# Performance work log

Measured on AMD Instinct MI355X. Metric: run time of the kernel, lower is better.

## Reference

```python
import jax, jax.numpy as jnp
import numpy as np

N_HEADS = 16
BLOCK_SIZE = 256


def _rope(x):
    # x: [B, H, L, d] ; matches torch RotaryPositionalEmbedding (interleave-split then concat)
    B, H, L, d = x.shape
    inv_freq = 1.0 / (10000.0 ** (jnp.arange(0, d, 2, dtype=jnp.float32) / d))
    t = jnp.arange(L, dtype=jnp.float32)[:, None] * inv_freq[None, :]  # [L, d/2]
    cos, sin = jnp.cos(t), jnp.sin(t)
    x1, x2 = x[..., 0::2], x[..., 1::2]
    return jnp.concatenate([x1 * cos - x2 * sin, x2 * cos + x1 * sin], axis=-1)


def setup_inputs() -> dict:
    key = jax.random.key(0)
    k1, k2, k3 = jax.random.split(key, 3)
    B, L, D = 2, 4096, 1024
    x = jax.random.normal(k1, (B, L, D), dtype=jnp.float32)
    Wqkv = jax.random.normal(k2, (3 * D, D), dtype=jnp.float32) * 0.02
    Wout = jax.random.normal(k3, (D, D), dtype=jnp.float32) * 0.02
    return {"x": x, "Wqkv": Wqkv, "Wout": Wout}


def reference(x, Wqkv, Wout):
    H, BS = N_HEADS, BLOCK_SIZE
    B, L, D = x.shape
    HD = D // H
    scale = HD ** (-0.5)
    nb = L // BS

    qkv = (x @ Wqkv.T).reshape(B, L, 3, H, HD).transpose(2, 0, 3, 1, 4)  # [3,B,H,L,HD]
    q, k, v = qkv[0], qkv[1], qkv[2]
    q, k = _rope(q), _rope(k)

    # block-diagonal causal attention: only within-block scores are ever unmasked,
    # and fp32 exp(finfo.min - max) == 0, so blockwise softmax == masked full softmax
    qb = q.reshape(B, H, nb, BS, HD)
    kb = k.reshape(B, H, nb, BS, HD)
    vb = v.reshape(B, H, nb, BS, HD)

    att = jnp.einsum('bhnqd,bhnkd->bhnqk', qb, kb) * scale
    causal = jnp.tril(jnp.ones((BS, BS), dtype=bool))
    att = jnp.where(causal, att, jnp.finfo(att.dtype).min)
    att = jax.nn.softmax(att, axis=-1)  # dropout p=0.0 -> identity

    out = jnp.einsum('bhnqk,bhnkd->bhnqd', att, vb)
    out = out.reshape(B, H, L, HD).transpose(0, 2, 1, 3).reshape(B, L, D)
    return out @ Wout.T
```

## Files before the change

### kernel.cpp

```cpp
#include <hip/hip_runtime.h>
#include <hip/hip_bf16.h>
#include <cstdint>
#include <cstddef>

typedef __hip_bfloat16 bf16;
typedef __attribute__((ext_vector_type(8))) short bf16x8;
typedef __attribute__((ext_vector_type(4))) float floatx4;

static constexpr int Bb = 2;
static constexpr int Ls = 4096;
static constexpr int Dm = 1024;
static constexpr int Hn = 16;
static constexpr int HD = 64;
static constexpr int BS = 256;
static constexpr int QKVROW = 3 * Dm;
static constexpr int KRP = 72;

static constexpr size_t NX  = (size_t)8192 * 1024;
static constexpr size_t NQ  = (size_t)8192 * 3072;
static constexpr size_t NW1 = (size_t)3072 * 1024;
static constexpr size_t NW2 = (size_t)1024 * 1024;

__device__ __forceinline__ void async_load16(const void* g, void* l) {
  __builtin_amdgcn_global_load_lds(
      (__attribute__((address_space(1))) void*)(void*)(g),
      (__attribute__((address_space(3))) void*)(l), 16, 0, 0);
}

__device__ __forceinline__ short f2bf(float f) {
  union { __hip_bfloat16 b; short s; } u;
  u.b = __float2bfloat16(f);
  return u.s;
}

__device__ __forceinline__ float bf2f(short s) {
  union { unsigned u; float f; } v;
  v.u = ((unsigned)(unsigned short)s) << 16;
  return v.f;
}

__device__ __forceinline__ bf16x8 load8(const float* p) {
  const float4 f0 = *(const float4*)(const void*)p;
  const float4 f1 = *(const float4*)(const void*)(p + 4);
  bf16x8 r;
  r[0] = f2bf(f0.x); r[1] = f2bf(f0.y); r[2] = f2bf(f0.z); r[3] = f2bf(f0.w);
  r[4] = f2bf(f1.x); r[5] = f2bf(f1.y); r[6] = f2bf(f1.z); r[7] = f2bf(f1.w);
  return r;
}

__device__ __forceinline__ void storeC(bf16* C, size_t idx, float v) {
  C[idx] = __float2bfloat16(v);
}
__device__ __forceinline__ void storeC(float* C, size_t idx, float v) {
  C[idx] = v;
}

__global__ void cvt3_kernel(const float* __restrict__ x, const float* __restrict__ w1,
                            const float* __restrict__ w2, bf16* __restrict__ xb,
                            bf16* __restrict__ w1b, bf16* __restrict__ w2b) {
  const size_t i = ((size_t)blockIdx.x * 256 + threadIdx.x) * 8;
  if (i < NX) {
    *(bf16x8*)(void*)((short*)(void*)xb + i) = load8(x + i);
  } else if (i < NX + NW1) {
    const size_t k = i - NX;
    *(bf16x8*)(void*)((short*)(void*)w1b + k) = load8(w1 + k);
  } else {
    const size_t k = i - NX - NW1;
    *(bf16x8*)(void*)((short*)(void*)w2b + k) = load8(w2 + k);
  }
}

template <typename TC>
__global__ __launch_bounds__(512, 2) void gemm_8p(
    const bf16* __restrict__ A, const bf16* __restrict__ Bm, TC* __restrict__ C,
    int M, int N, int K) {
  constexpr int BK = 64;
  __shared__ __align__(16) short sA[3][256 * 64];
  __shared__ __align__(16) short sB[3][128 * 64];
  const int tid = threadIdx.x;
  const int wave = tid >> 6, lane = tid & 63;
  const int quad = lane >> 4, l15 = lane & 15;
  const int wr = wave >> 1, wc = wave & 1;
  const int tm = blockIdx.y * 256, tn = blockIdx.x * 128;

  const int iLo = tid >> 3;
  const int csP = tid & 7;
  const int csL = csP ^ (iLo & 7);
  const bf16* gA[4];
  const bf16* gB[2];
#pragma unroll
  for (int j = 0; j < 4; j++) gA[j] = A + (size_t)(tm + iLo + 64 * j) * K + csL * 8;
#pragma unroll
  for (int j = 0; j < 2; j++) gB[j] = Bm + (size_t)(tn + iLo + 64 * j) * K + csL * 8;

  short* aC  = &sA[0][0];
  short* aN1 = &sA[1][0];
  short* aN2 = &sA[2][0];
  short* bC  = &sB[0][0];
  short* bN1 = &sB[1][0];
  short* bN2 = &sB[2][0];

#define STH1(aD, bD, kb)                                   \
  do {                                                     \
    async_load16(gA[0] + (kb), (aD) + tid * 8);            \
    async_load16(gA[1] + (kb), (aD) + 4096 + tid * 8);     \
    async_load16(gB[0] + (kb), (bD) + tid * 8);            \
  } while (0)
#define STH2(aD, bD, kb)                                   \
  do {                                                     \
    async_load16(gA[2] + (kb), (aD) + 8192 + tid * 8);     \
    async_load16(gA[3] + (kb), (aD) + 12288 + tid * 8);    \
    async_load16(gB[1] + (kb), (bD) + 4096 + tid * 8);     \
  } while (0)
#define BARR()                                             \
  do {                                                     \
    asm volatile("" ::: "memory");                         \
    __builtin_amdgcn_s_barrier();                          \
    asm volatile("" ::: "memory");                         \
  } while (0)
#define LGKM0() asm volatile("s_waitcnt lgkmcnt(0)" ::: "memory")
#define RDB4(bP)                                                               \
  do {                                                                         \
    _Pragma("unroll") for (int n = 0; n < 4; n++)                              \
        _Pragma("unroll") for (int ks = 0; ks < 2; ks++)                       \
            bfr[n][ks] = *(const bf16x8*)((bP) + (wc * 64 + n * 16 + l15) * 64 \
                              + ((ks * 4 + quad) ^ (l15 & 7)) * 8);            \
  } while (0)
#define RDA2(aP, mh)                                                           \
  do {                                                                         \
    _Pragma("unroll") for (int mm = 0; mm < 2; mm++)                           \
        _Pragma("unroll") for (int ks = 0; ks < 2; ks++)                       \
            af[mm][ks] = *(const bf16x8*)(                                     \
                (aP) + (wr * 64 + ((mh)*2 + mm) * 16 + l15) * 64               \
                + ((ks * 4 + quad) ^ (l15 & 7)) * 8);                          \
  } while (0)
#define MM16(mh)                                                               \
  do {                                                                         \
    __builtin_amdgcn_s_setprio(1);                                             \
    _Pragma("unroll") for (int mm = 0; mm < 2; mm++)                           \
        _Pragma("unroll") for (int n = 0; n < 4; n++) {                        \
      acc[(mh)*2 + mm][n] = __builtin_amdgcn_mfma_f32_16x16x32_bf16(           \
          af[mm][0], bfr[n][0], acc[(mh)*2 + mm][n], 0, 0, 0);                 \
      acc[(mh)*2 + mm][n] = __builtin_amdgcn_mfma_f32_16x16x32_bf16(           \
          af[mm][1], bfr[n][1], acc[(mh)*2 + mm][n], 0, 0, 0);                 \
    }                                                                          \
    __builtin_amdgcn_s_setprio(0);                                             \
  } while (0)

  floatx4 acc[4][4];
#pragma unroll
  for (int i = 0; i < 4; i++)
#pragma unroll
    for (int j = 0; j < 4; j++) acc[i][j] = {0.f, 0.f, 0.f, 0.f};
  bf16x8 af[2][2], bfr[4][2];

  const int nk = K / BK;

  STH1(aC, bC, 0);
  STH2(aC, bC, 0);
  STH1(aN1, bN1, BK);
  STH2(aN1, bN1, BK);
  asm volatile("s_waitcnt vmcnt(6)" ::: "memory");
  BARR();

  for (int t = 0; t < nk - 2; ++t) {
    const int kb2 = (t + 2) * BK;
    RDB4(bC);
    RDA2(aC, 0);
    STH1(aN2, bN2, kb2);
    BARR();
    LGKM0();
    MM16(0);
    BARR();
    RDA2(aC, 1);
    STH2(aN2, bN2, kb2);
    asm volatile("s_waitcnt vmcnt(6)" ::: "memory");
    BARR();
    LGKM0();
    MM16(1);
    BARR();
    short* ta = aC; aC = aN1; aN1 = aN2; aN2 = ta;
    short* tb = bC; bC = bN1; bN1 = bN2; bN2 = tb;
  }
  RDB4(bC);
  RDA2(aC, 0);
  BARR();
  LGKM0();
  MM16(0);
  BARR();
  RDA2(aC, 1);
  asm volatile("s_waitcnt vmcnt(0)" ::: "memory");
  BARR();
  LGKM0();
  MM16(1);
  BARR();
  {
    short* ta = aC; aC = aN1; aN1 = aN2; aN2 = ta;
    short* tb = bC; bC = bN1; bN1 = bN2; bN2 = tb;
  }
  RDB4(bC);
  RDA2(aC, 0);
  LGKM0();
  MM16(0);
  RDA2(aC, 1);
  LGKM0();
  MM16(1);
#undef STH1
#undef STH2
#undef BARR
#undef LGKM0
#undef RDB4
#undef RDA2
#undef MM16

#pragma unroll
  for (int m = 0; m < 4; m++)
#pragma unroll
    for (int n = 0; n < 4; n++)
#pragma unroll
      for (int r = 0; r < 4; r++) {
        const int row = tm + wr * 64 + m * 16 + quad * 4 + r;
        const int col = tn + wc * 64 + n * 16 + l15;
        storeC(C, (size_t)row * N + col, acc[m][n][r]);
      }
}

__device__ __forceinline__ void rope_frag(const bf16* __restrict__ row, int quad,
                                          float l_pos, const float* __restrict__ freq8,
                                          bf16x8* f0, bf16x8* f1) {
  const bf16x8 w0 = *(const bf16x8*)(const void*)(row + quad * 16);
  const bf16x8 w1 = *(const bf16x8*)(const void*)(row + quad * 16 + 8);
#pragma unroll
  for (int j = 0; j < 8; j++) {
    const short s1 = (j < 4) ? w0[2 * j] : w1[2 * (j - 4)];
    const short s2 = (j < 4) ? w0[2 * j + 1] : w1[2 * (j - 4) + 1];
    const float x1 = bf2f(s1), x2 = bf2f(s2);
    const float rev = l_pos * freq8[j];
    const float fr = rev - floorf(rev);
    const float c = __builtin_amdgcn_cosf(fr);
    const float s = __builtin_amdgcn_sinf(fr);
    (*f0)[j] = f2bf(x1 * c - x2 * s);
    (*f1)[j] = f2bf(x2 * c + x1 * s);
  }
}

__global__ __launch_bounds__(256) void attn_kernel(const bf16* __restrict__ qkv,
                                                   bf16* __restrict__ aout) {
  constexpr float SCALE = 0.125f;
  constexpr float LOG2E = 1.4426950408889634f;
  constexpr float INV2PI = 0.15915494309189535f;
  __shared__ __align__(16) short vT[HD * BS];
  __shared__ __align__(16) short kR[BS * KRP];
  __shared__ __align__(16) short pS[4][16 * 64];
  const int blk = blockIdx.x, h = blockIdx.y, b = blockIdx.z;
  const int tid = threadIdx.x;
  const int wave = tid >> 6, lane = tid & 63;
  const int quad = lane >> 4, l15 = lane & 15;
  const size_t row0 = (size_t)(b * Ls + blk * BS);
  const bf16* qkvR = qkv + row0 * QKVROW;

  float freq8[8];
#pragma unroll
  for (int j = 0; j < 8; j++)
    freq8[j] = exp2f(-13.287712379549449f * (float)(2 * (quad * 8 + j)) * (1.0f / 64.0f))
               * INV2PI;

  {
    const bf16* vrow = qkvR + (size_t)tid * QKVROW + 2 * Dm + h * HD;
#pragma unroll
    for (int i = 0; i < 8; i++) {
      bf16x8 vv = *(const bf16x8*)(vrow + i * 8);
#pragma unroll
      for (int e = 0; e < 8; e++) vT[(i * 8 + e) * BS + tid] = vv[e];
    }
  }

  {
    const bf16* krow = qkvR + (size_t)tid * QKVROW + Dm + h * HD;
    bf16x8 kw[8];
#pragma unroll
    for (int t = 0; t < 8; t++) kw[t] = *(const bf16x8*)(krow + t * 8);
    const float pos = (float)(blk * BS + tid);
    short tmp[64];
#pragma unroll
    for (int i = 0; i < 32; i++) {
      const float x1 = bf2f(kw[(2 * i) >> 3][(2 * i) & 7]);
      const float x2 = bf2f(kw[(2 * i + 1) >> 3][(2 * i + 1) & 7]);
      const float fq = exp2f(-13.287712379549449f * (float)(2 * i) * (1.0f / 64.0f)) * INV2PI;
      const float rev = pos * fq;
      const float fr = rev - floorf(rev);
      const float c = __builtin_amdgcn_cosf(fr);
      const float s = __builtin_amdgcn_sinf(fr);
      tmp[i]      = f2bf(x1 * c - x2 * s);
      tmp[i + 32] = f2bf(x2 * c + x1 * s);
    }
#pragma unroll
    for (int t = 0; t < 8; t++)
      *(bf16x8*)(kR + tid * KRP + t * 8) = *(const bf16x8*)(tmp + t * 8);
  }
  __syncthreads();

  short* myP = &pS[wave][0];

  for (int sp = 0; sp < 2; sp++) {
    const int s = sp ? (7 - wave) : wave;
    const int qrow0 = s * 32;
    const int kcmax = s >> 1;

    bf16x8 qf[2][2];
#pragma unroll
    for (int mt = 0; mt < 2; mt++) {
      const int qr = qrow0 + mt * 16 + l15;
      rope_frag(qkvR + (size_t)qr * QKVROW + h * HD, quad,
                (float)(blk * BS + qr), freq8, &qf[mt][0], &qf[mt][1]);
    }

    float m_i[2][4], l_i[2][4];
    floatx4 o[2][4];
#pragma unroll
    for (int mt = 0; mt < 2; mt++)
#pragma unroll
      for (int r = 0; r < 4; r++) { m_i[mt][r] = -1e30f; l_i[mt][r] = 0.f; }
#pragma unroll
    for (int mt = 0; mt < 2; mt++)
#pragma unroll
      for (int nt = 0; nt < 4; nt++) o[mt][nt] = {0.f, 0.f, 0.f, 0.f};

    for (int kc = 0; kc <= kcmax; kc++) {
      floatx4 sc[2][4];
#pragma unroll
      for (int mt = 0; mt < 2; mt++)
#pragma unroll
        for (int nt = 0; nt < 4; nt++) sc[mt][nt] = {0.f, 0.f, 0.f, 0.f};

      bf16x8 kf[4][2];
#pragma unroll
      for (int nt = 0; nt < 4; nt++) {
        const short* kr = kR + (kc * 64 + nt * 16 + l15) * KRP;
        kf[nt][0] = *(const bf16x8*)(kr + quad * 8);
        kf[nt][1] = *(const bf16x8*)(kr + 32 + quad * 8);
      }

#pragma unroll
      for (int mt = 0; mt < 2; mt++)
#pragma unroll
        for (int nt = 0; nt < 4; nt++) {
          sc[mt][nt] = __builtin_amdgcn_mfma_f32_16x16x32_bf16(qf[mt][0], kf[nt][0], sc[mt][nt], 0, 0, 0);
          sc[mt][nt] = __builtin_amdgcn_mfma_f32_16x16x32_bf16(qf[mt][1], kf[nt][1], sc[mt][nt], 0, 0, 0);
        }

      const bool diag = (kc == kcmax);
#pragma unroll
      for (int mt = 0; mt < 2; mt++)
#pragma unroll
        for (int r = 0; r < 4; r++) {
          const int rowg = qrow0 + mt * 16 + quad * 4 + r;
          float cmax = -1e30f;
#pragma unroll
          for (int nt = 0; nt < 4; nt++) {
            float sv = sc[mt][nt][r] * SCALE;
            if (diag && (kc * 64 + nt * 16 + l15 > rowg)) sv = -1e30f;
            sc[mt][nt][r] = sv;
            cmax = fmaxf(cmax, sv);
          }
#pragma unroll
          for (int off = 1; off < 16; off <<= 1)
            cmax = fmaxf(cmax, __shfl_xor(cmax, off, 64));
          const float mold = m_i[mt][r];
          const float mnew = fmaxf(mold, cmax);
          const float alpha = exp2f((mold - mnew) * LOG2E);
          float rsum = 0.f;
#pragma unroll
          for (int nt = 0; nt < 4; nt++) {
            const float p = exp2f((sc[mt][nt][r] - mnew) * LOG2E);
            sc[mt][nt][r] = p;
            rsum += p;
          }
#pragma unroll
          for (int off = 1; off < 16; off <<= 1)
            rsum += __shfl_xor(rsum, off, 64);
          l_i[mt][r] = l_i[mt][r] * alpha + rsum;
          m_i[mt][r] = mnew;
#pragma unroll
          for (int nt = 0; nt < 4; nt++) o[mt][nt][r] *= alpha;
        }

      bf16x8 vf0[4], vf1[4];
#pragma unroll
      for (int nt = 0; nt < 4; nt++) {
        vf0[nt] = *(const bf16x8*)(vT + (nt * 16 + l15) * BS + kc * 64 + quad * 8);
        vf1[nt] = *(const bf16x8*)(vT + (nt * 16 + l15) * BS + kc * 64 + 32 + quad * 8);
      }

#pragma unroll
      for (int mt = 0; mt < 2; mt++) {
#pragma unroll
        for (int nt = 0; nt < 4; nt++)
#pragma unroll
          for (int r = 0; r < 4; r++)
            myP[(quad * 4 + r) * 64 + nt * 16 + l15] = f2bf(sc[mt][nt][r]);
        __asm__ __volatile__("s_waitcnt lgkmcnt(0)" ::: "memory");
        const bf16x8 pf0 = *(const bf16x8*)(myP + l15 * 64 + quad * 8);
        const bf16x8 pf1 = *(const bf16x8*)(myP + l15 * 64 + 32 + quad * 8);
#pragma unroll
        for (int nt = 0; nt < 4; nt++) {
          o[mt][nt] = __builtin_amdgcn_mfma_f32_16x16x32_bf16(pf0, vf0[nt], o[mt][nt], 0, 0, 0);
          o[mt][nt] = __builtin_amdgcn_mfma_f32_16x16x32_bf16(pf1, vf1[nt], o[mt][nt], 0, 0, 0);
        }
        __asm__ __volatile__("s_waitcnt lgkmcnt(0)" ::: "memory");
      }
    }

#pragma unroll
    for (int mt = 0; mt < 2; mt++)
#pragma unroll
      for (int r = 0; r < 4; r++) {
        const float inv = 1.0f / l_i[mt][r];
#pragma unroll
        for (int nt = 0; nt < 4; nt++) {
          const size_t m = row0 + qrow0 + mt * 16 + quad * 4 + r;
          aout[m * Dm + h * HD + nt * 16 + l15] = __float2bfloat16(o[mt][nt][r] * inv);
        }
      }
  }
}

extern "C" void kernel_launch(void* const* d_in, const int* in_sizes, int n_in,
                              void* d_out, int out_size, void* d_ws, size_t ws_size,
                              hipStream_t stream) {
  const float* x    = (const float*)d_in[0];
  const float* Wqkv = (const float*)d_in[1];
  const float* Wout = (const float*)d_in[2];
  float* out = (float*)d_out;

  bf16* xb    = (bf16*)d_ws;
  bf16* qkv   = xb + NX;
  bf16* Wqkvb = qkv + NQ;
  bf16* Woutb = Wqkvb + NW1;
  bf16* attnb = xb;

  cvt3_kernel<<<(NX + NW1 + NW2) / 2048, 256, 0, stream>>>(x, Wqkv, Wout, xb, Wqkvb, Woutb);

  gemm_8p<bf16>
      <<<dim3(3072 / 128, 8192 / 256), 512, 0, stream>>>(xb, Wqkvb, qkv, 8192, 3072, 1024);
  attn_kernel<<<dim3(Ls / BS, Hn, Bb), 256, 0, stream>>>(qkv, attnb);
  gemm_8p<float>
      <<<dim3(1024 / 128, 8192 / 256), 512, 0, stream>>>(attnb, Woutb, out, 8192, 1024, 1024);
}
```

Baseline: 214.2 us.

## Use 256x256-tile GEMM with split-phase pipelined loads for QKV projection

Adds a new GEMM kernel with a square 256x256 output tile per 512-thread block, laid out as 2x4 waves each owning a 128x64 sub-tile. The loop splits each K-step into four phases that interleave A/B LDS reads, async global-to-LDS staging and MFMA bursts, with B prefetched two steps ahead. The QKV projection now uses it. The larger tile raises arithmetic intensity and reuse of each loaded operand. The cost is higher register pressure, more barriers per step, and half as many blocks (384) across the GPU's compute units.

```diff
diff --git a/kernel.cpp b/kernel.cpp
--- a/kernel.cpp
+++ b/kernel.cpp
@@ -68,6 +68,156 @@
     const size_t k = i - NX - NW1;
     *(bf16x8*)(void*)((short*)(void*)w2b + k) = load8(w2 + k);
   }
+}
+
+template <typename TC>
+__global__ __launch_bounds__(512, 2) void gemm_sq(
+    const bf16* __restrict__ A, const bf16* __restrict__ Bm, TC* __restrict__ C,
+    int M, int N, int K) {
+  constexpr int BK = 64;
+  __shared__ __align__(16) short sA[2][2][128 * 64];
+  __shared__ __align__(16) short sB[2][2][128 * 64];
+  const int tid = threadIdx.x;
+  const int wave = tid >> 6, lane = tid & 63;
+  const int quad = lane >> 4, l15 = lane & 15;
+  const int wr = wave >> 2, wc = wave & 3;
+  const int tm = blockIdx.y * 256, tn = blockIdx.x * 256;
+
+  const int iLo = tid >> 3;
+  const int csP = tid & 7;
+  const int csL = csP ^ (iLo & 7);
+  const bf16* gA[2][2];
+  const bf16* gB[2][2];
+#pragma unroll
+  for (int h = 0; h < 2; h++)
+#pragma unroll
+    for (int j = 0; j < 2; j++) {
+      gA[h][j] = A + (size_t)(tm + h * 128 + iLo + 64 * j) * K + csL * 8;
+      gB[h][j] = Bm + (size_t)(tn + h * 128 + iLo + 64 * j) * K + csL * 8;
+    }
+
+#define STGA(buf, h, kb)                                       \
+  do {                                                         \
+    short* d_ = &sA[buf][h][0] + tid * 8;                      \
+    async_load16(gA[h][0] + (kb), d_);                         \
+    async_load16(gA[h][1] + (kb), d_ + 4096);                  \
+  } while (0)
+#define STGB(buf, h, kb)                                       \
+  do {                                                         \
+    short* d_ = &sB[buf][h][0] + tid * 8;                      \
+    async_load16(gB[h][0] + (kb), d_);                         \
+    async_load16(gB[h][1] + (kb), d_ + 4096);                  \
+  } while (0)
+#define BARR()                                                 \
+  do {                                                         \
+    asm volatile("" ::: "memory");                             \
+    __builtin_amdgcn_s_barrier();                              \
+    asm volatile("" ::: "memory");                             \
+  } while (0)
+#define LGKM0() asm volatile("s_waitcnt lgkmcnt(0)" ::: "memory")
+#define RDB8(buf)                                                              \
+  do {                                                                         \
+    const short* p_ = &sB[buf][wc >> 1][0];                                    \
+    _Pragma("unroll") for (int n = 0; n < 4; n++)                              \
+        _Pragma("unroll") for (int ks = 0; ks < 2; ks++)                       \
+            bfr[n][ks] = *(const bf16x8*)(                                     \
+                p_ + ((wc & 1) * 64 + n * 16 + l15) * 64                       \
+                + (((ks * 4 + quad) ^ (l15 & 7)) * 8));                        \
+  } while (0)
+#define RDA4(buf, q)                                                           \
+  do {                                                                         \
+    const short* p_ = &sA[buf][wr][0];                                         \
+    _Pragma("unroll") for (int mm = 0; mm < 2; mm++)                           \
+        _Pragma("unroll") for (int ks = 0; ks < 2; ks++)                       \
+            af[mm][ks] = *(const bf16x8*)(                                     \
+                p_ + ((q) * 32 + mm * 16 + l15) * 64                           \
+                + (((ks * 4 + quad) ^ (l15 & 7)) * 8));                        \
+  } while (0)
+#define MM16(q)                                                                \
+  do {                                                                         \
+    __builtin_amdgcn_s_setprio(1);                                             \
+    _Pragma("unroll") for (int mm = 0; mm < 2; mm++)                           \
+        _Pragma("unroll") for (int n = 0; n < 4; n++) {                        \
+      acc[(q)*2 + mm][n] = __builtin_amdgcn_mfma_f32_16x16x32_bf16(            \
+          af[mm][0], bfr[n][0], acc[(q)*2 + mm][n], 0, 0, 0);                  \
+      acc[(q)*2 + mm][n] = __builtin_amdgcn_mfma_f32_16x16x32_bf16(            \
+          af[mm][1], bfr[n][1], acc[(q)*2 + mm][n], 0, 0, 0);                  \
+    }                                                                          \
+    __builtin_amdgcn_s_setprio(0);                                             \
+  } while (0)
+
+  floatx4 acc[8][4];
+#pragma unroll
+  for (int i = 0; i < 8; i++)
+#pragma unroll
+    for (int j = 0; j < 4; j++) acc[i][j] = {0.f, 0.f, 0.f, 0.f};
+  bf16x8 af[2][2], bfr[4][2];
+
+  const int nk = K / BK;
+
+  STGA(0, 0, 0);
+  STGA(0, 1, 0);
+  STGB(0, 0, 0);
+  STGB(0, 1, 0);
+  STGB(1, 0, BK);
+  STGB(1, 1, BK);
+  asm volatile("s_waitcnt vmcnt(4)" ::: "memory");
+  BARR();
+
+  for (int T = 0; T < nk; ++T) {
+    const int buf = T & 1, nbuf = buf ^ 1;
+    const int kA = (T + 1) * BK, kB = (T + 2) * BK;
+    const bool stA = (T + 1) < nk, stB = (T + 2) < nk;
+    RDB8(buf);
+    RDA4(buf, 0);
+    if (stA) STGA(nbuf, 0, kA);
+    asm volatile("s_waitcnt lgkmcnt(8)" ::: "memory");
+    BARR();
+    LGKM0();
+    MM16(0);
+    BARR();
+    RDA4(buf, 1);
+    if (stA) STGA(nbuf, 1, kA);
+    BARR();
+    LGKM0();
+    MM16(1);
+    BARR();
+    RDA4(buf, 2);
+    if (stB) STGB(buf, 0, kB);
+    BARR();
+    LGKM0();
+    MM16(2);
+    BARR();
+    RDA4(buf, 3);
+    if (stB) {
+      STGB(buf, 1, kB);
+      asm volatile("s_waitcnt vmcnt(4)" ::: "memory");
+    } else if (stA) {
+      asm volatile("s_waitcnt vmcnt(0)" ::: "memory");
+    }
+    BARR();
+    LGKM0();
+    MM16(3);
+    BARR();
+  }
+#undef STGA
+#undef STGB
+#undef BARR
+#undef LGKM0
+#undef RDB8
+#undef RDA4
+#undef MM16
+
+#pragma unroll
+  for (int mq = 0; mq < 8; mq++)
+#pragma unroll
+    for (int n = 0; n < 4; n++)
+#pragma unroll
+      for (int r = 0; r < 4; r++) {
+        const int row = tm + wr * 128 + mq * 16 + quad * 4 + r;
+        const int col = tn + wc * 64 + n * 16 + l15;
+        storeC(C, (size_t)row * N + col, acc[mq][n][r]);
+      }
 }
 
 template <typename TC>
@@ -441,8 +591,8 @@
 
   cvt3_kernel<<<(NX + NW1 + NW2) / 2048, 256, 0, stream>>>(x, Wqkv, Wout, xb, Wqkvb, Woutb);
 
-  gemm_8p<bf16>
-      <<<dim3(3072 / 128, 8192 / 256), 512, 0, stream>>>(xb, Wqkvb, qkv, 8192, 3072, 1024);
+  gemm_sq<bf16>
+      <<<dim3(3072 / 256, 8192 / 256), 512, 0, stream>>>(xb, Wqkvb, qkv, 8192, 3072, 1024);
   attn_kernel<<<dim3(Ls / BS, Hn, Bb), 256, 0, stream>>>(qkv, attnb);
   gemm_8p<float>
       <<<dim3(1024 / 128, 8192 / 256), 512, 0, stream>>>(attnb, Woutb, out, 8192, 1024, 1024);
```

Result: slower. 221.2 us (+3.2%).

## Software-pipeline LDS fragment reads with double-buffered registers in GEMM main loop

Applied to the files above, without the earlier changes.

Restructures the GEMM main loop so that the LDS reads of the A and B fragments for the next half-tile or next K-tile are issued before the current MFMA block runs. Register fragments are double-buffered (afL/afH, bfrA/bfrB) and partial lgkmcnt waits replace full drains. The aim is to hide LDS read latency behind the matrix instructions and to remove the prologue and epilogue special cases. In exchange, register pressure rises under the 512x2 launch bound, and the tuned waitcnt values have to match the exact count of outstanding loads.

```diff
diff --git a/kernel.cpp b/kernel.cpp
--- a/kernel.cpp
+++ b/kernel.cpp
@@ -71,7 +71,7 @@
 }
 
 template <typename TC>
-__global__ __launch_bounds__(512, 2) void gemm_8p(
+__global__ __launch_bounds__(512, 2) void gemm_pl(
     const bf16* __restrict__ A, const bf16* __restrict__ Bm, TC* __restrict__ C,
     int M, int N, int K) {
   constexpr int BK = 64;
@@ -118,41 +118,67 @@
     __builtin_amdgcn_s_barrier();                          \
     asm volatile("" ::: "memory");                         \
   } while (0)
-#define LGKM0() asm volatile("s_waitcnt lgkmcnt(0)" ::: "memory")
-#define RDB4(bP)                                                               \
+#define RDB8(bP, DST)                                                          \
   do {                                                                         \
     _Pragma("unroll") for (int n = 0; n < 4; n++)                              \
         _Pragma("unroll") for (int ks = 0; ks < 2; ks++)                       \
-            bfr[n][ks] = *(const bf16x8*)((bP) + (wc * 64 + n * 16 + l15) * 64 \
+            DST[n][ks] = *(const bf16x8*)((bP) + (wc * 64 + n * 16 + l15) * 64 \
                               + ((ks * 4 + quad) ^ (l15 & 7)) * 8);            \
   } while (0)
-#define RDA2(aP, mh)                                                           \
+#define RDA2(aP, DST, mh)                                                      \
   do {                                                                         \
     _Pragma("unroll") for (int mm = 0; mm < 2; mm++)                           \
         _Pragma("unroll") for (int ks = 0; ks < 2; ks++)                       \
-            af[mm][ks] = *(const bf16x8*)(                                     \
+            DST[mm][ks] = *(const bf16x8*)(                                    \
                 (aP) + (wr * 64 + ((mh)*2 + mm) * 16 + l15) * 64               \
                 + ((ks * 4 + quad) ^ (l15 & 7)) * 8);                          \
   } while (0)
-#define MM16(mh)                                                               \
+#define MM16(AF, BF, mh)                                                       \
   do {                                                                         \
     __builtin_amdgcn_s_setprio(1);                                             \
     _Pragma("unroll") for (int mm = 0; mm < 2; mm++)                           \
         _Pragma("unroll") for (int n = 0; n < 4; n++) {                        \
       acc[(mh)*2 + mm][n] = __builtin_amdgcn_mfma_f32_16x16x32_bf16(           \
-          af[mm][0], bfr[n][0], acc[(mh)*2 + mm][n], 0, 0, 0);                 \
+          AF[mm][0], BF[n][0], acc[(mh)*2 + mm][n], 0, 0, 0);                  \
       acc[(mh)*2 + mm][n] = __builtin_amdgcn_mfma_f32_16x16x32_bf16(           \
-          af[mm][1], bfr[n][1], acc[(mh)*2 + mm][n], 0, 0, 0);                 \
+          AF[mm][1], BF[n][1], acc[(mh)*2 + mm][n], 0, 0, 0);                  \
     }                                                                          \
     __builtin_amdgcn_s_setprio(0);                                             \
   } while (0)
+#define TILE(t, BCUR, BNXT)                                                    \
+  do {                                                                         \
+                                                                  \
+    RDA2(aC, afH, 1);                                                          \
+    if ((t) + 2 < nk) STH1(aN2, bN2, ((t) + 2) * BK);                          \
+    if ((t) + 2 < nk)                                                          \
+      asm volatile("s_waitcnt vmcnt(3)" ::: "memory");                         \
+    else if ((t) + 1 < nk)                                                     \
+      asm volatile("s_waitcnt vmcnt(0)" ::: "memory");                         \
+    BARR();                                                                    \
+    asm volatile("s_waitcnt lgkmcnt(4)" ::: "memory");                         \
+    MM16(afL, BCUR, 0);                                                        \
+    BARR();                                                                    \
+                                                                  \
+    if ((t) + 1 < nk) {                                                        \
+      RDB8(bN1, BNXT);                                                         \
+      RDA2(aN1, afL, 0);                                                       \
+      if ((t) + 2 < nk) STH2(aN2, bN2, ((t) + 2) * BK);                        \
+      asm volatile("s_waitcnt lgkmcnt(12)" ::: "memory");                      \
+    } else {                                                                   \
+      asm volatile("s_waitcnt lgkmcnt(0)" ::: "memory");                       \
+    }                                                                          \
+    MM16(afH, BCUR, 1);                                                        \
+    BARR();                                                                    \
+    { short* ta_ = aC; aC = aN1; aN1 = aN2; aN2 = ta_; }                       \
+    { short* tb_ = bC; bC = bN1; bN1 = bN2; bN2 = tb_; }                       \
+  } while (0)
 
   floatx4 acc[4][4];
 #pragma unroll
   for (int i = 0; i < 4; i++)
 #pragma unroll
     for (int j = 0; j < 4; j++) acc[i][j] = {0.f, 0.f, 0.f, 0.f};
-  bf16x8 af[2][2], bfr[4][2];
+  bf16x8 afL[2][2], afH[2][2], bfrA[4][2], bfrB[4][2];
 
   const int nk = K / BK;
 
@@ -162,56 +188,20 @@
   STH2(aN1, bN1, BK);
   asm volatile("s_waitcnt vmcnt(6)" ::: "memory");
   BARR();
-
-  for (int t = 0; t < nk - 2; ++t) {
-    const int kb2 = (t + 2) * BK;
-    RDB4(bC);
-    RDA2(aC, 0);
-    STH1(aN2, bN2, kb2);
-    BARR();
-    LGKM0();
-    MM16(0);
-    BARR();
-    RDA2(aC, 1);
-    STH2(aN2, bN2, kb2);
-    asm volatile("s_waitcnt vmcnt(6)" ::: "memory");
-    BARR();
-    LGKM0();
-    MM16(1);
-    BARR();
-    short* ta = aC; aC = aN1; aN1 = aN2; aN2 = ta;
-    short* tb = bC; bC = bN1; bN1 = bN2; bN2 = tb;
-  }
-  RDB4(bC);
-  RDA2(aC, 0);
-  BARR();
-  LGKM0();
-  MM16(0);
-  BARR();
-  RDA2(aC, 1);
-  asm volatile("s_waitcnt vmcnt(0)" ::: "memory");
-  BARR();
-  LGKM0();
-  MM16(1);
-  BARR();
-  {
-    short* ta = aC; aC = aN1; aN1 = aN2; aN2 = ta;
-    short* tb = bC; bC = bN1; bN1 = bN2; bN2 = tb;
-  }
-  RDB4(bC);
-  RDA2(aC, 0);
-  LGKM0();
-  MM16(0);
-  RDA2(aC, 1);
-  LGKM0();
-  MM16(1);
+  RDB8(bC, bfrA);
+  RDA2(aC, afL, 0);
+
+  for (int t = 0; t < nk; t += 2) {
+    TILE(t, bfrA, bfrB);
+    TILE(t + 1, bfrB, bfrA);
+  }
 #undef STH1
 #undef STH2
 #undef BARR
-#undef LGKM0
-#undef RDB4
+#undef RDB8
 #undef RDA2
 #undef MM16
+#undef TILE
 
 #pragma unroll
   for (int m = 0; m < 4; m++)
@@ -441,9 +431,9 @@
 
   cvt3_kernel<<<(NX + NW1 + NW2) / 2048, 256, 0, stream>>>(x, Wqkv, Wout, xb, Wqkvb, Woutb);
 
-  gemm_8p<bf16>
+  gemm_pl<bf16>
       <<<dim3(3072 / 128, 8192 / 256), 512, 0, stream>>>(xb, Wqkvb, qkv, 8192, 3072, 1024);
   attn_kernel<<<dim3(Ls / BS, Hn, Bb), 256, 0, stream>>>(qkv, attnb);
-  gemm_8p<float>
+  gemm_pl<float>
       <<<dim3(1024 / 128, 8192 / 256), 512, 0, stream>>>(attnb, Woutb, out, 8192, 1024, 1024);
 }
```

New measurement: 219.4 us. 1.02x slower.
